# Kernel tuning notes

Hardware: AMD Instinct MI355X
Metric: run time of the kernel (lower is better)

The kernel has to match this reference:

```python
import jax, jax.numpy as jnp
import numpy as np

NUM_HEADS = 16
HEAD_DIM = 64
HIDDEN = NUM_HEADS * HEAD_DIM  # 1024
BATCH, SEQ = 4, 2048


def setup_inputs() -> dict:
    key = jax.random.key(0)
    k1, k2, k3, k4 = jax.random.split(key, 4)
    hidden_states = jax.random.normal(k1, (BATCH, SEQ, HIDDEN), dtype=jnp.float32)
    attention_mask = jnp.arange(SEQ)[None, :] < int(SEQ * 0.9)
    attention_mask = jnp.broadcast_to(attention_mask, (BATCH, SEQ))
    s_in = 1.0 / np.sqrt(HIDDEN)
    Wqkv = jax.random.normal(k2, (HIDDEN, 3 * HIDDEN), dtype=jnp.float32) * s_in
    Wout = jax.random.normal(k3, (HIDDEN, HIDDEN), dtype=jnp.float32) * s_in
    bout = jnp.zeros((HIDDEN,), dtype=jnp.float32)
    return {"hidden_states": hidden_states, "attention_mask": attention_mask,
            "Wqkv": Wqkv, "Wout": Wout, "bout": bout}


def reference(hidden_states, attention_mask, Wqkv, Wout, bout):
    B, S, H = hidden_states.shape
    qkv = hidden_states @ Wqkv  # [B,S,3*H]
    qkv = qkv.reshape(B, S, 3, NUM_HEADS, HEAD_DIM)
    qkv = jnp.transpose(qkv, (2, 0, 3, 1, 4))  # [3,B,nh,S,hd]
    q, k, v = qkv[0], qkv[1], qkv[2]
    scale = 1.0 / jnp.sqrt(jnp.float32(HEAD_DIM))
    attn = jnp.einsum('bhid,bhjd->bhij', q, k) * scale  # [B,nh,S,S]
    bias = jnp.where(attention_mask[:, None, None, :], 0.0,
                     jnp.finfo(jnp.float32).min)
    attn = attn + bias
    attn = jax.nn.softmax(attn, axis=-1)
    out = jnp.einsum('bhij,bhjd->bhid', attn, v)  # [B,nh,S,hd]
    out = jnp.transpose(out, (0, 2, 1, 3)).reshape(B, S, H)
    return out @ Wout + bout
```

## Files before the change

### kernel.cpp

```cpp
#include <hip/hip_runtime.h>


typedef short bh8 __attribute__((ext_vector_type(8)));
typedef short bh4 __attribute__((ext_vector_type(4)));
typedef float f32x4 __attribute__((ext_vector_type(4)));

#define B_ 4
#define S_ 2048
#define NH_ 16
#define HD_ 64
#define H_ 1024

__device__ float g_biasf[B_ * S_];
__device__ int g_tl[B_ * 33];

__device__ inline short f2bf(float f) {
    unsigned u = __builtin_bit_cast(unsigned, f);
    u = (u + 0x7fffu + ((u >> 16) & 1u)) >> 16;
    return (short)u;
}

__device__ inline unsigned pk2bf(float a, float b) {
#if __has_builtin(__builtin_amdgcn_cvt_pk_bf16_f32)
    auto r = __builtin_amdgcn_cvt_pk_bf16_f32(a, b);
    return __builtin_bit_cast(unsigned, r);
#else
    unsigned ua = __builtin_bit_cast(unsigned, a) + 0x8000u;
    unsigned ub = __builtin_bit_cast(unsigned, b) + 0x8000u;
    return __builtin_amdgcn_perm(ub, ua, 0x07060302);
#endif
}

__global__ void prep_all(const float* __restrict__ hidden, const float* __restrict__ Wqkv,
                         const float* __restrict__ Wout, const int* __restrict__ mask,
                         short* __restrict__ Xbf, short* __restrict__ WqkvT,
                         short* __restrict__ WoutT, float qs) {
    __shared__ float tile[32][33];
    int bi = blockIdx.x, tid = threadIdx.x;

    if (bi < 8192) {
        int i = (bi * 256 + tid) * 4;
        float4 v = *(const float4*)(hidden + i);
        union { short s[4]; unsigned long long u; } r;
        r.s[0] = f2bf(v.x); r.s[1] = f2bf(v.y); r.s[2] = f2bf(v.z); r.s[3] = f2bf(v.w);
        *(unsigned long long*)(Xbf + i) = r.u;
        return;
    }
    if (bi < 12288) {
        const float* in; short* out; int N, qcols, idx;
        if (bi < 11264) { in = Wqkv; out = WqkvT; N = 3 * H_; qcols = H_; idx = bi - 8192;
        } else          { in = Wout; out = WoutT; N = H_;    qcols = 0;  idx = bi - 11264; }
        int xt = (bi < 11264) ? 96 : 32;
        int n0 = (idx % xt) * 32, k0 = (idx / xt) * 32;
        int tx = tid & 31, ty = tid >> 5;
#pragma unroll
        for (int i = 0; i < 32; i += 8)
            tile[ty + i][tx] = in[(long)(k0 + ty + i) * N + n0 + tx];
        __syncthreads();
#pragma unroll
        for (int i = 0; i < 32; i += 8) {
            int n = n0 + ty + i;
            float v = tile[tx][ty + i];
            if (n < qcols) v *= qs;
            out[(long)n * H_ + k0 + tx] = f2bf(v);
        }
        return;
    }
    if (bi < 12320) {
        int i = (bi - 12288) * 256 + tid;
        g_biasf[i] = mask[i] ? 0.0f : -1e30f;
        return;
    }
    {
        int b = bi - 12320;
        if (tid < 64) {
            int t = tid, flag = 0;
            if (t < 32) {
                bool anyA = false, anyM = false;
                for (int i = 0; i < 64; ++i) {
                    int m = mask[b * S_ + t * 64 + i];
                    anyA |= (m != 0); anyM |= (m == 0);
                }
                flag = anyA ? (anyM ? 1 : 2) : 0;
            }
            unsigned long long act = __ballot(flag != 0);
            int pos = __popcll(act & ((1ull << t) - 1ull));
            if (flag) g_tl[b * 33 + 1 + pos] = t | (flag << 16);
            if (t == 0) g_tl[b * 33] = __popcll(act);
        }
    }
}

__global__ __launch_bounds__(256, 2) void gemm_bf16(
    const short* __restrict__ A, const short* __restrict__ Bt,
    int M, int N, int K, int mode,
    short* __restrict__ qk, short* __restrict__ vt,
    const float* __restrict__ bias, float* __restrict__ out) {
    __shared__ short smem[128 * 136];
    short* sA[2] = { smem, smem + 4096 };
    short* sB[2] = { smem + 8192, smem + 12288 };
    int tid = threadIdx.x;
    int lane = tid & 63, wid = tid >> 6;
    int quad = lane >> 4, l15 = lane & 15;
    int wy = wid >> 1, wx = wid & 1;
    int m0 = blockIdx.y * 128, n0 = blockIdx.x * 128;

    f32x4 acc[4][4] = {};
    const short* Ag = A + (long)m0 * K;
    const short* Bg = Bt + (long)n0 * K;

    for (int k0 = 0; k0 < K; k0 += 64) {
#pragma unroll
        for (int half = 0; half < 2; ++half) {
#pragma unroll
            for (int i = 0; i < 2; ++i) {
                int flat = i * 256 + tid;
                int r = flat >> 2, c = (flat & 3) << 3;
                __builtin_amdgcn_global_load_lds(
                    (const __attribute__((address_space(1))) void*)(Ag + (long)r * K + k0 + half * 32 + c),
                    (__attribute__((address_space(3))) void*)(sA[half] + i * 2048 + wid * 512),
                    16, 0, 0);
                __builtin_amdgcn_global_load_lds(
                    (const __attribute__((address_space(1))) void*)(Bg + (long)r * K + k0 + half * 32 + c),
                    (__attribute__((address_space(3))) void*)(sB[half] + i * 2048 + wid * 512),
                    16, 0, 0);
            }
        }
        __syncthreads();
#pragma unroll
        for (int half = 0; half < 2; ++half) {
            bh8 af[4], bfr[4];
#pragma unroll
            for (int mi = 0; mi < 4; ++mi)
                af[mi] = *(const bh8*)(sA[half] + (wy * 64 + mi * 16 + l15) * 32 + quad * 8);
#pragma unroll
            for (int ni = 0; ni < 4; ++ni)
                bfr[ni] = *(const bh8*)(sB[half] + (wx * 64 + ni * 16 + l15) * 32 + quad * 8);
#pragma unroll
            for (int mi = 0; mi < 4; ++mi)
#pragma unroll
                for (int ni = 0; ni < 4; ++ni)
                    acc[mi][ni] = __builtin_amdgcn_mfma_f32_16x16x32_bf16(af[mi], bfr[ni], acc[mi][ni], 0, 0, 0);
        }
        __syncthreads();
    }

    if (mode == 0) {
        bool isV = (n0 >= 2048);
#pragma unroll
        for (int mi = 0; mi < 4; ++mi)
#pragma unroll
            for (int ni = 0; ni < 4; ++ni) {
                int c = wx * 64 + ni * 16 + l15;
                int rb = wy * 64 + mi * 16 + quad * 4;
                if (isV) {
                    unsigned lo = pk2bf(acc[mi][ni][0], acc[mi][ni][1]);
                    unsigned hi = pk2bf(acc[mi][ni][2], acc[mi][ni][3]);
                    uint2 uu = {lo, hi};
                    *(bh4*)(smem + c * 136 + rb) = __builtin_bit_cast(bh4, uu);
                } else {
#pragma unroll
                    for (int reg = 0; reg < 4; ++reg)
                        smem[(rb + reg) * 136 + c] = f2bf(acc[mi][ni][reg]);
                }
            }
        __syncthreads();
        int b = m0 >> 11, sbase = m0 & 2047;
#pragma unroll
        for (int j = 0; j < 8; ++j) {
            int f = (j * 256 + tid) * 8;
            int i0 = f >> 7, i1 = f & 127;
            bh8 v = *(const bh8*)(smem + i0 * 136 + i1);
            if (isV) {
                int cc = n0 - 2048 + i0;
                int h = cc >> 6, d = cc & 63;
                *(bh8*)(vt + ((long)(b * NH_ + h) * HD_ + d) * S_ + sbase + i1) = v;
            } else {
                *(bh8*)(qk + (long)(m0 + i0) * 2048 + n0 + i1) = v;
            }
        }
    } else {
#pragma unroll
        for (int mi = 0; mi < 4; ++mi)
#pragma unroll
            for (int ni = 0; ni < 4; ++ni) {
                int gc = n0 + wx * 64 + ni * 16 + l15;
                float bv = bias[gc];
#pragma unroll
                for (int reg = 0; reg < 4; ++reg) {
                    int gr = m0 + wy * 64 + mi * 16 + quad * 4 + reg;
                    out[(long)gr * N + gc] = acc[mi][ni][reg] + bv;
                }
            }
    }
}

__device__ inline void ld_tile(const short* __restrict__ Kb, const short* __restrict__ Vb,
                               int j0, int tid, bh8* kp, bh8* vp) {
#pragma unroll
    for (int i = 0; i < 2; ++i) {
        int flat = i * 256 + tid;
        int r = flat >> 3, c = (flat & 7) << 3;
        kp[i] = *(const bh8*)(Kb + (long)(j0 + r) * 2048 + c);
        vp[i] = *(const bh8*)(Vb + (long)r * S_ + j0 + c);
    }
}
__device__ inline void st_tile(short* lk, short* lv, int tid, const bh8* kp, const bh8* vp) {
#pragma unroll
    for (int i = 0; i < 2; ++i) {
        int flat = i * 256 + tid;
        int r = flat >> 3, c = (flat & 7) << 3;
        *(bh8*)(lk + r * 72 + c) = kp[i];
        *(bh8*)(lv + r * 72 + c) = vp[i];
    }
}

__global__ __launch_bounds__(256, 2) void attn_fwd(
    const short* __restrict__ QK, const short* __restrict__ Vtw,
    short* __restrict__ Aout) {
    __shared__ short lK[2][64 * 72];
    __shared__ short lV[2][64 * 72];
    int tid = threadIdx.x;
    int lane = tid & 63, w = tid >> 6;
    int quad = lane >> 4, l15 = lane & 15;
    int p = blockIdx.x;
    int b = p >> 4, h = p & 15;
    int qbase = blockIdx.y * 256 + w * 64;

    const short* Kb = QK + (long)b * S_ * 2048 + 1024 + h * HD_;
    const short* Vb = Vtw + (long)p * HD_ * S_;

    bh8 qf[4][2];
#pragma unroll
    for (int mi = 0; mi < 4; ++mi)
#pragma unroll
        for (int ks = 0; ks < 2; ++ks)
            qf[mi][ks] = *(const bh8*)(QK + (long)(b * S_ + qbase + mi * 16 + l15) * 2048
                                       + h * HD_ + ks * 32 + quad * 8);

    f32x4 o[4][4] = {};
    f32x4 ls[4] = {};
    const bh8 ones = {0x3F80, 0x3F80, 0x3F80, 0x3F80, 0x3F80, 0x3F80, 0x3F80, 0x3F80};

    int cnt = g_tl[b * 33];
    int e0 = g_tl[b * 33 + 1];
    int j0 = (e0 & 0xffff) << 6, flag = e0 >> 16;
    bh8 kp[2], vp[2];
    ld_tile(Kb, Vb, j0, tid, kp, vp);
    st_tile(lK[0], lV[0], tid, kp, vp);
    int cur = 0;

    for (int it = 0; it < cnt; ++it) {
        __syncthreads();
        bool more = (it + 1 < cnt);
        int nj0 = 0, nflag = 0;
        if (more) {
            int en = g_tl[b * 33 + 2 + it];
            nj0 = (en & 0xffff) << 6; nflag = en >> 16;
            ld_tile(Kb, Vb, nj0, tid, kp, vp);
        }
        const short* ck = lK[cur];
        const short* cv = lV[cur];

        bh4 pf[4][4];
#pragma unroll
        for (int nj = 0; nj < 4; ++nj) {
            f32x4 scn[4] = {};
#pragma unroll
            for (int ks = 0; ks < 2; ++ks) {
                bh8 kf = *(const bh8*)(ck + (nj * 16 + l15) * 72 + ks * 32 + quad * 8);
#pragma unroll
                for (int mi = 0; mi < 4; ++mi)
                    scn[mi] = __builtin_amdgcn_mfma_f32_16x16x32_bf16(kf, qf[mi][ks], scn[mi], 0, 0, 0);
            }
            if (flag == 1) {
                f32x4 bb = *(const f32x4*)(g_biasf + b * S_ + j0 + nj * 16 + quad * 4);
#pragma unroll
                for (int mi = 0; mi < 4; ++mi) {
#pragma unroll
                    for (int r = 0; r < 4; ++r) scn[mi][r] += bb[r];
                }
            }
#pragma unroll
            for (int mi = 0; mi < 4; ++mi) {
                unsigned u0 = pk2bf(__builtin_amdgcn_exp2f(scn[mi][0]),
                                    __builtin_amdgcn_exp2f(scn[mi][1]));
                unsigned u1 = pk2bf(__builtin_amdgcn_exp2f(scn[mi][2]),
                                    __builtin_amdgcn_exp2f(scn[mi][3]));
                uint2 uu = {u0, u1};
                pf[nj][mi] = __builtin_bit_cast(bh4, uu);
            }
        }

#pragma unroll
        for (int pr = 0; pr < 2; ++pr) {
            int njA = 2 * pr, njB = 2 * pr + 1;
            bh8 a[4];
#pragma unroll
            for (int mi = 0; mi < 4; ++mi)
                a[mi] = __builtin_shufflevector(pf[njA][mi], pf[njB][mi], 0, 1, 2, 3, 4, 5, 6, 7);
#pragma unroll
            for (int mi = 0; mi < 4; ++mi)
                ls[mi] = __builtin_amdgcn_mfma_f32_16x16x32_bf16(a[mi], ones, ls[mi], 0, 0, 0);
#pragma unroll
            for (int nd = 0; nd < 4; ++nd) {
                bh4 v0 = *(const bh4*)(cv + (nd * 16 + l15) * 72 + njA * 16 + quad * 4);
                bh4 v1 = *(const bh4*)(cv + (nd * 16 + l15) * 72 + njB * 16 + quad * 4);
                bh8 vf = __builtin_shufflevector(v0, v1, 0, 1, 2, 3, 4, 5, 6, 7);
#pragma unroll
                for (int mi = 0; mi < 4; ++mi)
                    o[mi][nd] = __builtin_amdgcn_mfma_f32_16x16x32_bf16(a[mi], vf, o[mi][nd], 0, 0, 0);
            }
        }

        if (more) st_tile(lK[cur ^ 1], lV[cur ^ 1], tid, kp, vp);
        j0 = nj0; flag = nflag; cur ^= 1;
    }

#pragma unroll
    for (int mi = 0; mi < 4; ++mi)
#pragma unroll
        for (int reg = 0; reg < 4; ++reg) {
            float inv = __builtin_amdgcn_rcpf(ls[mi][reg]);
            int s = qbase + mi * 16 + quad * 4 + reg;
#pragma unroll
            for (int nd = 0; nd < 4; ++nd) {
                int col = h * HD_ + nd * 16 + l15;
                Aout[((long)b * S_ + s) * H_ + col] = f2bf(o[mi][nd][reg] * inv);
            }
        }
}

extern "C" void kernel_launch(void* const* d_in, const int* in_sizes, int n_in,
                              void* d_out, int out_size, void* d_ws, size_t ws_size,
                              hipStream_t stream) {
    const float* hidden = (const float*)d_in[0];
    const int* mask = (const int*)d_in[1];
    const float* Wqkv = (const float*)d_in[2];
    const float* Wout = (const float*)d_in[3];
    const float* bout = (const float*)d_in[4];
    float* out = (float*)d_out;

    char* ws = (char*)d_ws;
    const size_t XBF = 0;
    const size_t WQKVT = 16777216;
    const size_t WOUTT = WQKVT + 6291456;
    const size_t QKO = WOUTT + 2097152;
    const size_t VT = QKO + 33554432;

    short* Xbf = (short*)(ws + XBF);
    short* WqkvT = (short*)(ws + WQKVT);
    short* WoutT = (short*)(ws + WOUTT);
    short* QK = (short*)(ws + QKO);
    short* Vt = (short*)(ws + VT);
    short* Aout = Xbf;

    const float Cs = 0.18033688011112042f;

    prep_all<<<dim3(12324), dim3(256), 0, stream>>>(
        hidden, Wqkv, Wout, mask, Xbf, WqkvT, WoutT, Cs);

    gemm_bf16<<<dim3(24, 64), dim3(256), 0, stream>>>(
        Xbf, WqkvT, B_ * S_, 3 * H_, H_, 0, QK, Vt, nullptr, nullptr);

    attn_fwd<<<dim3(64, 8), dim3(256), 0, stream>>>(QK, Vt, Aout);

    gemm_bf16<<<dim3(8, 64), dim3(256), 0, stream>>>(
        Aout, WoutT, B_ * S_, H_, H_, 1, nullptr, nullptr, bout, out);
}
```

Before: 250.6 us.

## Load K/V MFMA fragments directly from global memory, drop LDS staging

Removes the shared-memory double buffer for K and V tiles and the per-iteration block barrier. Each wave now loads its own K and V MFMA fragments straight from global memory (relying on L1/L2 caching), and raises wave priority around the MFMA sequences with s_setprio. This avoids LDS traffic and __syncthreads, but all four waves fetch the same K/V data redundantly from cache. Global-load latency is no longer hidden by explicit prefetching.

```diff
diff --git a/kernel.cpp b/kernel.cpp
--- a/kernel.cpp
+++ b/kernel.cpp
@@ -195,31 +195,9 @@
     }
 }
 
-__device__ inline void ld_tile(const short* __restrict__ Kb, const short* __restrict__ Vb,
-                               int j0, int tid, bh8* kp, bh8* vp) {
-#pragma unroll
-    for (int i = 0; i < 2; ++i) {
-        int flat = i * 256 + tid;
-        int r = flat >> 3, c = (flat & 7) << 3;
-        kp[i] = *(const bh8*)(Kb + (long)(j0 + r) * 2048 + c);
-        vp[i] = *(const bh8*)(Vb + (long)r * S_ + j0 + c);
-    }
-}
-__device__ inline void st_tile(short* lk, short* lv, int tid, const bh8* kp, const bh8* vp) {
-#pragma unroll
-    for (int i = 0; i < 2; ++i) {
-        int flat = i * 256 + tid;
-        int r = flat >> 3, c = (flat & 7) << 3;
-        *(bh8*)(lk + r * 72 + c) = kp[i];
-        *(bh8*)(lv + r * 72 + c) = vp[i];
-    }
-}
-
 __global__ __launch_bounds__(256, 2) void attn_fwd(
     const short* __restrict__ QK, const short* __restrict__ Vtw,
     short* __restrict__ Aout) {
-    __shared__ short lK[2][64 * 72];
-    __shared__ short lV[2][64 * 72];
     int tid = threadIdx.x;
     int lane = tid & 63, w = tid >> 6;
     int quad = lane >> 4, l15 = lane & 15;
@@ -227,8 +205,9 @@
     int b = p >> 4, h = p & 15;
     int qbase = blockIdx.y * 256 + w * 64;
 
-    const short* Kb = QK + (long)b * S_ * 2048 + 1024 + h * HD_;
-    const short* Vb = Vtw + (long)p * HD_ * S_;
+    const short* Kf = QK + (long)b * S_ * 2048 + 1024 + h * HD_
+                      + (long)l15 * 2048 + quad * 8;
+    const short* Vf = Vtw + (long)p * HD_ * S_ + (long)l15 * S_ + quad * 4;
 
     bh8 qf[4][2];
 #pragma unroll
@@ -243,36 +222,26 @@
     const bh8 ones = {0x3F80, 0x3F80, 0x3F80, 0x3F80, 0x3F80, 0x3F80, 0x3F80, 0x3F80};
 
     int cnt = g_tl[b * 33];
-    int e0 = g_tl[b * 33 + 1];
-    int j0 = (e0 & 0xffff) << 6, flag = e0 >> 16;
-    bh8 kp[2], vp[2];
-    ld_tile(Kb, Vb, j0, tid, kp, vp);
-    st_tile(lK[0], lV[0], tid, kp, vp);
-    int cur = 0;
-
     for (int it = 0; it < cnt; ++it) {
-        __syncthreads();
-        bool more = (it + 1 < cnt);
-        int nj0 = 0, nflag = 0;
-        if (more) {
-            int en = g_tl[b * 33 + 2 + it];
-            nj0 = (en & 0xffff) << 6; nflag = en >> 16;
-            ld_tile(Kb, Vb, nj0, tid, kp, vp);
-        }
-        const short* ck = lK[cur];
-        const short* cv = lV[cur];
+        int e = g_tl[b * 33 + 1 + it];
+        int j0 = (e & 0xffff) << 6, flag = e >> 16;
+        const short* Kt = Kf + (long)j0 * 2048;
+        const short* Vt_ = Vf + j0;
 
         bh4 pf[4][4];
 #pragma unroll
         for (int nj = 0; nj < 4; ++nj) {
             f32x4 scn[4] = {};
-#pragma unroll
-            for (int ks = 0; ks < 2; ++ks) {
-                bh8 kf = *(const bh8*)(ck + (nj * 16 + l15) * 72 + ks * 32 + quad * 8);
-#pragma unroll
-                for (int mi = 0; mi < 4; ++mi)
-                    scn[mi] = __builtin_amdgcn_mfma_f32_16x16x32_bf16(kf, qf[mi][ks], scn[mi], 0, 0, 0);
-            }
+            bh8 kf0 = *(const bh8*)(Kt + (long)(nj * 16) * 2048);
+            bh8 kf1 = *(const bh8*)(Kt + (long)(nj * 16) * 2048 + 32);
+            __builtin_amdgcn_s_setprio(1);
+#pragma unroll
+            for (int mi = 0; mi < 4; ++mi)
+                scn[mi] = __builtin_amdgcn_mfma_f32_16x16x32_bf16(kf0, qf[mi][0], scn[mi], 0, 0, 0);
+#pragma unroll
+            for (int mi = 0; mi < 4; ++mi)
+                scn[mi] = __builtin_amdgcn_mfma_f32_16x16x32_bf16(kf1, qf[mi][1], scn[mi], 0, 0, 0);
+            __builtin_amdgcn_s_setprio(0);
             if (flag == 1) {
                 f32x4 bb = *(const f32x4*)(g_biasf + b * S_ + j0 + nj * 16 + quad * 4);
 #pragma unroll
@@ -299,22 +268,21 @@
 #pragma unroll
             for (int mi = 0; mi < 4; ++mi)
                 a[mi] = __builtin_shufflevector(pf[njA][mi], pf[njB][mi], 0, 1, 2, 3, 4, 5, 6, 7);
+            __builtin_amdgcn_s_setprio(1);
 #pragma unroll
             for (int mi = 0; mi < 4; ++mi)
                 ls[mi] = __builtin_amdgcn_mfma_f32_16x16x32_bf16(a[mi], ones, ls[mi], 0, 0, 0);
 #pragma unroll
             for (int nd = 0; nd < 4; ++nd) {
-                bh4 v0 = *(const bh4*)(cv + (nd * 16 + l15) * 72 + njA * 16 + quad * 4);
-                bh4 v1 = *(const bh4*)(cv + (nd * 16 + l15) * 72 + njB * 16 + quad * 4);
+                bh4 v0 = *(const bh4*)(Vt_ + (long)(nd * 16) * S_ + njA * 16);
+                bh4 v1 = *(const bh4*)(Vt_ + (long)(nd * 16) * S_ + njB * 16);
                 bh8 vf = __builtin_shufflevector(v0, v1, 0, 1, 2, 3, 4, 5, 6, 7);
 #pragma unroll
                 for (int mi = 0; mi < 4; ++mi)
                     o[mi][nd] = __builtin_amdgcn_mfma_f32_16x16x32_bf16(a[mi], vf, o[mi][nd], 0, 0, 0);
             }
-        }
-
-        if (more) st_tile(lK[cur ^ 1], lV[cur ^ 1], tid, kp, vp);
-        j0 = nj0; flag = nflag; cur ^= 1;
+            __builtin_amdgcn_s_setprio(0);
+        }
     }
 
 #pragma unroll
```

Result: slower. 343.5 us (+37.1%).
